# Performance work log

Measured on AMD Instinct MI355X. Metric: run time of the kernel, lower is better.

Reference implementation:

```python
import jax, jax.numpy as jnp
import numpy as np

EPS = 1e-5


def sage_conv(x, src, dst, Wl, Wr, b, n):
    # PyG SAGEConv: out_i = W_l * mean_{j in N(i)} x_j + W_r * x_i + b
    agg = jax.ops.segment_sum(x[src], dst, num_segments=n)  # [N, d]
    deg = jax.ops.segment_sum(jnp.ones_like(src, dtype=x.dtype), dst, num_segments=n)
    agg = agg / jnp.maximum(deg, 1.0)[:, None]
    return agg @ Wl + x @ Wr + b


def setup_inputs() -> dict:
    key = jax.random.key(0)
    ks = jax.random.split(key, 12)
    N, E, D_IN, D_H, D_OUT = 50000, 600000, 128, 128, 64
    x = jax.random.normal(ks[0], (N, D_IN), dtype=jnp.float32)
    edge_index = jax.random.randint(ks[1], (2, E), 0, N, dtype=jnp.int64)
    s_in = 1.0 / np.sqrt(D_IN)
    s_h = 1.0 / np.sqrt(D_H)
    return {
        "x": x,
        "edge_index": edge_index,
        "Wl0": jax.random.normal(ks[2], (D_IN, D_H), jnp.float32) * s_in,
        "Wr0": jax.random.normal(ks[3], (D_IN, D_H), jnp.float32) * s_in,
        "b0": jnp.zeros((D_H,), jnp.float32),
        "Wl1": jax.random.normal(ks[4], (D_H, D_H), jnp.float32) * s_h,
        "Wr1": jax.random.normal(ks[5], (D_H, D_H), jnp.float32) * s_h,
        "b1": jnp.zeros((D_H,), jnp.float32),
        "Wl2": jax.random.normal(ks[6], (D_H, D_OUT), jnp.float32) * s_h,
        "Wr2": jax.random.normal(ks[7], (D_H, D_OUT), jnp.float32) * s_h,
        "b2": jnp.zeros((D_OUT,), jnp.float32),
        "gamma": jnp.ones((D_H,), jnp.float32),
        "beta": jnp.zeros((D_H,), jnp.float32),
    }


def reference(x, edge_index, Wl0, Wr0, b0, Wl1, Wr1, b1, Wl2, Wr2, b2, gamma, beta):
    n = x.shape[0]
    src, dst = edge_index[0], edge_index[1]
    residual = x  # in_channels == hidden_channels -> no residual_transform
    # layer 0: conv + relu (+ dropout as identity in eval)
    h = jax.nn.relu(sage_conv(x, src, dst, Wl0, Wr0, b0, n))
    # middle layer: conv + BN(batch stats) + relu + residual
    h = sage_conv(h, src, dst, Wl1, Wr1, b1, n)
    mu = jnp.mean(h, axis=0)
    var = jnp.var(h, axis=0)  # biased, as in torch BN normalization
    h = (h - mu) * jax.lax.rsqrt(var + EPS) * gamma + beta
    h = jax.nn.relu(h) + residual
    # output layer
    h = sage_conv(h, src, dst, Wl2, Wr2, b2, n)
    return jax.nn.log_softmax(h, axis=-1)
```

## Files before the change

### kernel.cpp

```cpp
#include <hip/hip_runtime.h>
#include <hip/hip_bf16.h>


#define WS_EPS 1e-5f

typedef unsigned short ushort_t;
typedef unsigned int uint_t;
typedef unsigned char uchar_t;
typedef ushort_t ushort8 __attribute__((ext_vector_type(8)));
typedef short short8 __attribute__((ext_vector_type(8)));
typedef float f32x4 __attribute__((ext_vector_type(4)));
typedef _Float16 half2v __attribute__((ext_vector_type(2)));

__device__ __forceinline__ float bf2f(ushort_t u) {
    return __uint_as_float(((uint_t)u) << 16);
}
__device__ __forceinline__ ushort_t f2bf(float f) {
    uint_t u = __float_as_uint(f);
    u = (u + 0x7fffu + ((u >> 16) & 1u)) >> 16;
    return (ushort_t)u;
}
__device__ __forceinline__ uchar_t f2e4m3(float f) {
    _Float16 hf = (_Float16)f;
    uint_t h = (uint_t)__builtin_bit_cast(unsigned short, hf);
    uint_t s = (h >> 8) & 0x80u;
    uint_t r = h & 0x7fffu;
    if (r < 0x2400u) return (uchar_t)0;
    if (r > 0x5F40u) r = 0x5F00u;
    uint_t u = r - 0x2000u;
    uint_t m = (u + 0x3fu + ((u >> 7) & 1u)) >> 7;
    return (uchar_t)(s | m);
}

constexpr int SCHUNK = 4096;

__global__ __launch_bounds__(256) void k_scan_part(const int* __restrict__ deg,
                                                   int* __restrict__ bsum, int n) {
    int t = threadIdx.x;
    int base = blockIdx.x * SCHUNK + t * 16;
    int s = 0;
#pragma unroll
    for (int j = 0; j < 16; ++j) {
        int i = base + j;
        if (i < n) s += deg[i];
    }
#pragma unroll
    for (int d = 1; d < 64; d <<= 1) s += __shfl_xor(s, d);
    __shared__ int wt[4];
    if ((t & 63) == 0) wt[t >> 6] = s;
    __syncthreads();
    if (t == 0) bsum[blockIdx.x] = wt[0] + wt[1] + wt[2] + wt[3];
}

__global__ __launch_bounds__(64) void k_scan_bsum(const int* __restrict__ bsum,
                                                  int* __restrict__ boff,
                                                  int* __restrict__ off_n, int nb) {
    int lane = threadIdx.x;
    int carry = 0;
    for (int base = 0; base < nb; base += 64) {
        int t = base + lane;
        int v = (t < nb) ? bsum[t] : 0;
        int x = v;
#pragma unroll
        for (int d = 1; d < 64; d <<= 1) {
            int y = __shfl_up(x, d);
            if (lane >= d) x += y;
        }
        if (t < nb) boff[t] = carry + x - v;
        carry += __shfl(x, 63);
    }
    if (lane == 0) *off_n = carry;
}

__global__ __launch_bounds__(256) void k_scan_apply(const int* __restrict__ deg,
                                                    const int* __restrict__ boff,
                                                    int* __restrict__ off, int n) {
    int t = threadIdx.x;
    int lane = t & 63, wid = t >> 6;
    int base = blockIdx.x * SCHUNK + t * 16;
    int v[16];
    int s = 0;
#pragma unroll
    for (int j = 0; j < 16; ++j) {
        int i = base + j;
        v[j] = (i < n) ? deg[i] : 0;
        s += v[j];
    }
    int x = s;
#pragma unroll
    for (int d = 1; d < 64; d <<= 1) {
        int y = __shfl_up(x, d);
        if (lane >= d) x += y;
    }
    __shared__ int wtot[4];
    if (lane == 63) wtot[wid] = x;
    __syncthreads();
    int woff = 0;
    for (int wj = 0; wj < wid; ++wj) woff += wtot[wj];
    int run = boff[blockIdx.x] + woff + x - s;
#pragma unroll
    for (int j = 0; j < 16; ++j) {
        int i = base + j;
        if (i < n) off[i] = run;
        run += v[j];
    }
}

__global__ __launch_bounds__(256) void k_scatter(const int* __restrict__ ei,
                                                 const int* __restrict__ off,
                                                 int* __restrict__ cur,
                                                 int* __restrict__ csr, int E) {
    int e = blockIdx.x * 256 + threadIdx.x;
    if (e < E) {
        int d = ei[E + e];
        int s = ei[e];
        int p = atomicAdd(&cur[d], 1);
        csr[off[d] + p] = s;
    }
}

__global__ __launch_bounds__(256) void k_deg_prep(const int* __restrict__ ei,
                                                  int* __restrict__ deg, int E, int eb,
                                                  const float* __restrict__ x,
                                                  ushort_t* __restrict__ xb,
                                                  uchar_t* __restrict__ x8,
                                                  int total2, int nb_cvt,
                                                  const float* __restrict__ Wl0,
                                                  const float* __restrict__ Wr0,
                                                  const float* __restrict__ Wl1,
                                                  const float* __restrict__ Wr1,
                                                  const float* __restrict__ Wl2,
                                                  const float* __restrict__ Wr2,
                                                  ushort_t* __restrict__ wts) {
    int b = blockIdx.x;
    if (b < eb) {
        int e = b * 256 + threadIdx.x;
        if (e < E) atomicAdd(&deg[ei[E + e]], 1);
        return;
    }
    b -= eb;
    if (b < nb_cvt) {
        int i = b * 256 + threadIdx.x;
        if (i >= total2) return;
        float2 v = *(const float2*)&x[(size_t)i * 2];
        uint_t p = (uint_t)f2bf(v.x) | ((uint_t)f2bf(v.y) << 16);
        *(uint_t*)&xb[(size_t)i * 2] = p;
        ushort_t q = (ushort_t)((uint_t)f2e4m3(v.x) | ((uint_t)f2e4m3(v.y) << 8));
        *(ushort_t*)&x8[(size_t)i * 2] = q;
        return;
    }
    int id = (b - nb_cvt) * 256 + threadIdx.x;
    if (id >= 81920) return;
    const float* W;
    int rel, nout, base;
    if (id < 65536) {
        int m = id >> 14;
        rel = id & 16383;
        nout = 128;
        base = m << 14;
        W = (m == 0) ? Wl0 : (m == 1) ? Wr0 : (m == 2) ? Wl1 : Wr1;
    } else {
        int m = (id - 65536) >> 13;
        rel = (id - 65536) & 8191;
        nout = 64;
        base = 65536 + (m << 13);
        W = (m == 0) ? Wl2 : Wr2;
    }
    int c = rel >> 7;
    int k = rel & 127;
    wts[base + rel] = f2bf(W[(size_t)k * nout + c]);
}

constexpr int LDK = 136;

template <int EPI>
__global__ __launch_bounds__(256, 2) void k_dgemm(const ushort_t* __restrict__ X1,
                                                  const ushort_t* __restrict__ W1,
                                                  const ushort_t* __restrict__ X2,
                                                  const ushort_t* __restrict__ W2,
                                                  const float* __restrict__ bias,
                                                  ushort_t* __restrict__ outp,
                                                  uchar_t* __restrict__ out8,
                                                  float* __restrict__ stats, int n) {
    constexpr int K = 128, NOUT = 128;
    __shared__ ushort_t Bs[2 * 64 * LDK];

    const int t = threadIdx.x;
    const int lane = t & 63;
    const int r16 = lane & 15, kb = lane >> 4;
    const int colbase = (blockIdx.x & 1) * 64;

#pragma unroll
    for (int u = 0; u < 8; ++u) {
        int f = u * 256 + t;
        int rel = f & 1023;
        int col = rel >> 4, seg = rel & 15;
        const ushort_t* Wm = (u < 4) ? W1 : W2;
        *(ushort8*)&Bs[(u < 4 ? 0 : 1) * 64 * LDK + col * LDK + seg * 8] =
            *(const ushort8*)&Wm[(size_t)(colbase + col) * K + seg * 8];
    }
    __syncthreads();

    float bcol[4];
#pragma unroll
    for (int fn = 0; fn < 4; ++fn) bcol[fn] = bias[colbase + fn * 16 + r16];
    float ssum[4] = {0.f, 0.f, 0.f, 0.f}, qsum[4] = {0.f, 0.f, 0.f, 0.f};

    const int strips = (n + 15) >> 4;
    const int wstr = (gridDim.x >> 1) * 4;
    const int s0 = (blockIdx.x >> 1) * 4 + (t >> 6);

    auto loadA = [&](short8* a, int s) {
        int arow = s * 16 + r16;
        bool ok = arow < n;
        size_t xo = (size_t)arow * K + kb * 8;
#pragma unroll
        for (int ks = 0; ks < 4; ++ks)
            a[ks] = ok ? *(const short8*)&X1[xo + ks * 32] : (short8)0;
#pragma unroll
        for (int ks = 0; ks < 4; ++ks)
            a[4 + ks] = ok ? *(const short8*)&X2[xo + ks * 32] : (short8)0;
    };

    auto work = [&](const short8* a, int s) {
        f32x4 acc[4] = {(f32x4)0.f, (f32x4)0.f, (f32x4)0.f, (f32x4)0.f};
#pragma unroll
        for (int ks = 0; ks < 4; ++ks) {
#pragma unroll
            for (int fn = 0; fn < 4; ++fn) {
                short8 b = *(const short8*)&Bs[(fn * 16 + r16) * LDK + ks * 32 + kb * 8];
                acc[fn] = __builtin_amdgcn_mfma_f32_16x16x32_bf16(a[ks], b, acc[fn], 0, 0, 0);
            }
        }
#pragma unroll
        for (int ks = 0; ks < 4; ++ks) {
#pragma unroll
            for (int fn = 0; fn < 4; ++fn) {
                short8 b = *(const short8*)&Bs[64 * LDK + (fn * 16 + r16) * LDK + ks * 32 + kb * 8];
                acc[fn] = __builtin_amdgcn_mfma_f32_16x16x32_bf16(a[4 + ks], b, acc[fn], 0, 0, 0);
            }
        }
        int rb = s * 16 + kb * 4;
#pragma unroll
        for (int r = 0; r < 4; ++r) {
            int row = rb + r;
            if (row >= n) continue;
#pragma unroll
            for (int fn = 0; fn < 4; ++fn) {
                int col = colbase + fn * 16 + r16;
                float v = acc[fn][r] + bcol[fn];
                if constexpr (EPI == 2) {
                    float rv = fmaxf(v, 0.f);
                    outp[(size_t)row * NOUT + col] = f2bf(rv);
                    out8[(size_t)row * NOUT + col] = f2e4m3(rv);
                } else {
                    outp[(size_t)row * NOUT + col] = f2bf(v);
                    ssum[fn] += v;
                    qsum[fn] += v * v;
                }
            }
        }
    };

    short8 aA[8], aB[8], aC[8];
    int s = s0;
    if (s < strips) {
        loadA(aA, s);
        int sB = s + wstr;
        bool vB = sB < strips;
        if (vB) loadA(aB, sB);
        for (;;) {
            int sC = sB + wstr;
            bool vC = vB && (sC < strips);
            if (vC) loadA(aC, sC);
            work(aA, s);
            if (!vB) break;
            int sD = sC + wstr;
            bool vD = vC && (sD < strips);
            if (vD) loadA(aA, sD);
            work(aB, sB);
            if (!vC) break;
            int sE = sD + wstr;
            bool vE = vD && (sE < strips);
            if (vE) loadA(aB, sE);
            work(aC, sC);
            if (!vD) break;
            s = sD;
            sB = sE;
            vB = vE;
        }
    }

    if constexpr (EPI == 1) {
#pragma unroll
        for (int fn = 0; fn < 4; ++fn) {
            ssum[fn] += __shfl_xor(ssum[fn], 16);
            ssum[fn] += __shfl_xor(ssum[fn], 32);
            qsum[fn] += __shfl_xor(qsum[fn], 16);
            qsum[fn] += __shfl_xor(qsum[fn], 32);
        }
        if (kb == 0) {
#pragma unroll
            for (int fn = 0; fn < 4; ++fn) {
                int col = colbase + fn * 16 + r16;
                atomicAdd(&stats[col], ssum[fn]);
                atomicAdd(&stats[128 + col], qsum[fn]);
            }
        }
    }
}

__global__ __launch_bounds__(256, 2) void k_cgemm(const ushort_t* __restrict__ H,
                                                  const ushort_t* __restrict__ WL,
                                                  const ushort_t* __restrict__ WR,
                                                  const float* __restrict__ b2,
                                                  ushort_t* __restrict__ A64,
                                                  ushort_t* __restrict__ Tb, int n) {
    constexpr int K = 128;
    __shared__ ushort_t Bs[2 * 64 * LDK];

    const int t = threadIdx.x;
    const int lane = t & 63;
    const int r16 = lane & 15, kb = lane >> 4;

#pragma unroll
    for (int u = 0; u < 8; ++u) {
        int f = u * 256 + t;
        int rel = f & 1023;
        int col = rel >> 4, seg = rel & 15;
        const ushort_t* Wm = (u < 4) ? WL : WR;
        *(ushort8*)&Bs[(u < 4 ? 0 : 1) * 64 * LDK + col * LDK + seg * 8] =
            *(const ushort8*)&Wm[(size_t)col * K + seg * 8];
    }
    __syncthreads();

    float bcol[4];
#pragma unroll
    for (int fn = 0; fn < 4; ++fn) bcol[fn] = b2[fn * 16 + r16];

    const int strips = (n + 15) >> 4;
    const int wstr = gridDim.x * 4;
    const int s0 = blockIdx.x * 4 + (t >> 6);

    auto loadA = [&](short8* a, int s) {
        int arow = s * 16 + r16;
        bool ok = arow < n;
        size_t xo = (size_t)arow * K + kb * 8;
#pragma unroll
        for (int ks = 0; ks < 4; ++ks)
            a[ks] = ok ? *(const short8*)&H[xo + ks * 32] : (short8)0;
    };

    auto work = [&](const short8* a, int s) {
        f32x4 aL[4] = {(f32x4)0.f, (f32x4)0.f, (f32x4)0.f, (f32x4)0.f};
        f32x4 aR[4] = {(f32x4)0.f, (f32x4)0.f, (f32x4)0.f, (f32x4)0.f};
#pragma unroll
        for (int ks = 0; ks < 4; ++ks) {
#pragma unroll
            for (int fn = 0; fn < 4; ++fn) {
                short8 bl = *(const short8*)&Bs[(fn * 16 + r16) * LDK + ks * 32 + kb * 8];
                short8 br = *(const short8*)&Bs[64 * LDK + (fn * 16 + r16) * LDK + ks * 32 + kb * 8];
                aL[fn] = __builtin_amdgcn_mfma_f32_16x16x32_bf16(a[ks], bl, aL[fn], 0, 0, 0);
                aR[fn] = __builtin_amdgcn_mfma_f32_16x16x32_bf16(a[ks], br, aR[fn], 0, 0, 0);
            }
        }
        int rb = s * 16 + kb * 4;
#pragma unroll
        for (int r = 0; r < 4; ++r) {
            int row = rb + r;
            if (row >= n) continue;
#pragma unroll
            for (int fn = 0; fn < 4; ++fn) {
                int col = fn * 16 + r16;
                A64[(size_t)row * 64 + col] = f2bf(aL[fn][r]);
                Tb[(size_t)row * 64 + col] = f2bf(aR[fn][r] + bcol[fn]);
            }
        }
    };

    short8 aA[4], aB[4], aC[4];
    int s = s0;
    if (s < strips) {
        loadA(aA, s);
        int sB = s + wstr;
        bool vB = sB < strips;
        if (vB) loadA(aB, sB);
        for (;;) {
            int sC = sB + wstr;
            bool vC = vB && (sC < strips);
            if (vC) loadA(aC, sC);
            work(aA, s);
            if (!vB) break;
            int sD = sC + wstr;
            bool vD = vC && (sD < strips);
            if (vD) loadA(aA, sD);
            work(aB, sB);
            if (!vC) break;
            int sE = sD + wstr;
            bool vE = vD && (sE < strips);
            if (vE) loadA(aB, sE);
            work(aC, sC);
            if (!vD) break;
            s = sD;
            sB = sE;
            vB = vE;
        }
    }
}

__global__ __launch_bounds__(256) void k_segmean8(const uchar_t* __restrict__ U8,
                                                  const int* __restrict__ off,
                                                  const int* __restrict__ srcs,
                                                  ushort_t* __restrict__ out, int n) {
    int node = blockIdx.x * 32 + (threadIdx.x >> 3);
    int sub = threadIdx.x & 7;
    if (node >= n) return;
    int beg = off[node], end = off[node + 1];
    half2v aE0 = (half2v)0, aE1 = (half2v)0, aE2 = (half2v)0, aE3 = (half2v)0;
    half2v aO0 = (half2v)0, aO1 = (half2v)0, aO2 = (half2v)0, aO3 = (half2v)0;

#define DEC(dw, AE, AO)                                                           \
    {                                                                             \
        uint_t xe = (dw)&0x00ff00ffu;                                             \
        uint_t xo = ((dw) >> 8) & 0x00ff00ffu;                                    \
        uint_t he = ((xe & 0x00800080u) << 8) |                                   \
                    (((xe & 0x007f007fu) << 7) + 0x20002000u);                    \
        uint_t ho = ((xo & 0x00800080u) << 8) |                                   \
                    (((xo & 0x007f007fu) << 7) + 0x20002000u);                    \
        AE += __builtin_bit_cast(half2v, he);                                     \
        AO += __builtin_bit_cast(half2v, ho);                                     \
    }

    auto addrow = [&](int sidx) {
        uint4 v = *(const uint4*)&U8[(size_t)sidx * 128 + sub * 16];
        DEC(v.x, aE0, aO0)
        DEC(v.y, aE1, aO1)
        DEC(v.z, aE2, aO2)
        DEC(v.w, aE3, aO3)
    };
#undef DEC

    int i = beg;
    for (; i + 8 <= end; i += 8) {
        int sv[8];
#pragma unroll
        for (int u = 0; u < 8; ++u) sv[u] = srcs[i + u];
#pragma unroll
        for (int u = 0; u < 8; ++u) addrow(sv[u]);
    }
    for (; i < end; ++i) addrow(srcs[i]);

    int d = end - beg;
    float inv = 1.f / (float)(d > 1 ? d : 1);
    ushort8 o0, o1;
#define PACK(AE, AO, O, IDX)                     \
    O[IDX] = f2bf((float)AE[0] * inv);           \
    O[IDX + 1] = f2bf((float)AO[0] * inv);       \
    O[IDX + 2] = f2bf((float)AE[1] * inv);       \
    O[IDX + 3] = f2bf((float)AO[1] * inv);
    PACK(aE0, aO0, o0, 0)
    PACK(aE1, aO1, o0, 4)
    PACK(aE2, aO2, o1, 0)
    PACK(aE3, aO3, o1, 4)
#undef PACK
    *(ushort8*)&out[(size_t)node * 128 + sub * 16] = o0;
    *(ushort8*)&out[(size_t)node * 128 + sub * 16 + 8] = o1;
}

__global__ __launch_bounds__(256) void k_segmean_lsm(const ushort_t* __restrict__ A64,
                                                     const int* __restrict__ off,
                                                     const int* __restrict__ srcs,
                                                     const ushort_t* __restrict__ Tb,
                                                     float* __restrict__ out, int n) {
    int node = blockIdx.x * 32 + (threadIdx.x >> 3);
    int sub = threadIdx.x & 7;
    if (node >= n) return;
    int beg = off[node], end = off[node + 1];
    float a[8];
#pragma unroll
    for (int j = 0; j < 8; ++j) a[j] = 0.f;
    int i = beg;
    for (; i + 8 <= end; i += 8) {
        int sv[8];
#pragma unroll
        for (int u = 0; u < 8; ++u) sv[u] = srcs[i + u];
#pragma unroll
        for (int u = 0; u < 8; ++u) {
            ushort8 v = *(const ushort8*)&A64[(size_t)sv[u] * 64 + sub * 8];
#pragma unroll
            for (int j = 0; j < 8; ++j) a[j] += bf2f((ushort_t)v[j]);
        }
    }
    for (; i < end; ++i) {
        ushort8 v = *(const ushort8*)&A64[(size_t)srcs[i] * 64 + sub * 8];
#pragma unroll
        for (int j = 0; j < 8; ++j) a[j] += bf2f((ushort_t)v[j]);
    }
    int d = end - beg;
    float inv = 1.f / (float)(d > 1 ? d : 1);
    ushort8 tv = *(const ushort8*)&Tb[(size_t)node * 64 + sub * 8];
    float vv[8];
#pragma unroll
    for (int j = 0; j < 8; ++j) vv[j] = a[j] * inv + bf2f((ushort_t)tv[j]);
    float m = vv[0];
#pragma unroll
    for (int j = 1; j < 8; ++j) m = fmaxf(m, vv[j]);
#pragma unroll
    for (int dd = 1; dd < 8; dd <<= 1) m = fmaxf(m, __shfl_xor(m, dd));
    float e = 0.f;
#pragma unroll
    for (int j = 0; j < 8; ++j) e += expf(vv[j] - m);
#pragma unroll
    for (int dd = 1; dd < 8; dd <<= 1) e += __shfl_xor(e, dd);
    float lg = m + logf(e);
    f32x4 o0, o1;
#pragma unroll
    for (int j = 0; j < 4; ++j) {
        o0[j] = vv[j] - lg;
        o1[j] = vv[4 + j] - lg;
    }
    *(f32x4*)&out[(size_t)node * 64 + sub * 8] = o0;
    *(f32x4*)&out[(size_t)node * 64 + sub * 8 + 4] = o1;
}

__global__ __launch_bounds__(256) void k_bnapply(const ushort_t* __restrict__ P,
                                                 const ushort_t* __restrict__ Xb,
                                                 const float* __restrict__ stats,
                                                 const float* __restrict__ gamma,
                                                 const float* __restrict__ beta,
                                                 ushort_t* __restrict__ H, int n) {
    int i = blockIdx.x * 256 + threadIdx.x;
    if (i >= n * 64) return;
    int nd = i >> 6;
    int c = (i & 63) << 1;
    float inv_n = 1.f / (float)n;
    float mu0 = stats[c] * inv_n, mu1 = stats[c + 1] * inv_n;
    float v0 = stats[128 + c] * inv_n - mu0 * mu0;
    float v1 = stats[128 + c + 1] * inv_n - mu1 * mu1;
    float s0 = rsqrtf(v0 + WS_EPS) * gamma[c];
    float s1 = rsqrtf(v1 + WS_EPS) * gamma[c + 1];
    uint_t pv = *(const uint_t*)&P[(size_t)nd * 128 + c];
    uint_t xv = *(const uint_t*)&Xb[(size_t)nd * 128 + c];
    float p0 = __uint_as_float(pv << 16);
    float p1 = __uint_as_float(pv & 0xffff0000u);
    float x0 = __uint_as_float(xv << 16);
    float x1 = __uint_as_float(xv & 0xffff0000u);
    float h0 = fmaxf((p0 - mu0) * s0 + beta[c], 0.f) + x0;
    float h1 = fmaxf((p1 - mu1) * s1 + beta[c + 1], 0.f) + x1;
    uint_t pk = (uint_t)f2bf(h0) | ((uint_t)f2bf(h1) << 16);
    *(uint_t*)&H[(size_t)nd * 128 + c] = pk;
}

extern "C" void kernel_launch(void* const* d_in, const int* in_sizes, int n_in,
                              void* d_out, int out_size, void* d_ws, size_t ws_size,
                              hipStream_t stream) {
    const float* x     = (const float*)d_in[0];
    const int*   ei    = (const int*)d_in[1];
    const float* Wl0   = (const float*)d_in[2];
    const float* Wr0   = (const float*)d_in[3];
    const float* b0    = (const float*)d_in[4];
    const float* Wl1   = (const float*)d_in[5];
    const float* Wr1   = (const float*)d_in[6];
    const float* b1    = (const float*)d_in[7];
    const float* Wl2   = (const float*)d_in[8];
    const float* Wr2   = (const float*)d_in[9];
    const float* b2    = (const float*)d_in[10];
    const float* gamma = (const float*)d_in[11];
    const float* beta  = (const float*)d_in[12];

    const int n = in_sizes[0] / 128;
    const int E = in_sizes[1] / 2;
    const int nb_scan = (n + SCHUNK - 1) / SCHUNK;

    char* w = (char*)d_ws;
    auto alloc = [&](size_t bytes) -> void* {
        void* p = (void*)w;
        w += (bytes + 255) & ~(size_t)255;
        return p;
    };
    int*      deg   = (int*)alloc((size_t)n * 4);
    int*      cur   = (int*)alloc((size_t)n * 4);
    float*    stats = (float*)alloc(256 * 4);
    size_t    zbytes = (size_t)((char*)w - (char*)deg);
    int*      off   = (int*)alloc(((size_t)n + 1) * 4);
    int*      csr   = (int*)alloc((size_t)E * 4);
    int*      bsum  = (int*)alloc(256 * 4);
    int*      boff  = (int*)alloc(256 * 4);
    ushort_t* wts   = (ushort_t*)alloc((size_t)81920 * 2);
    ushort_t* xb    = (ushort_t*)alloc((size_t)n * 128 * 2);
    uchar_t*  x8    = (uchar_t*)alloc((size_t)n * 128);
    ushort_t* H     = (ushort_t*)alloc((size_t)n * 128 * 2);
    uchar_t*  H8    = (uchar_t*)alloc((size_t)n * 128);
    ushort_t* Pb    = (ushort_t*)alloc((size_t)n * 128 * 2);
    ushort_t* M     = (ushort_t*)alloc((size_t)n * 128 * 2);
    ushort_t* A64   = (ushort_t*)alloc((size_t)n * 64 * 2);
    ushort_t* Tb    = (ushort_t*)alloc((size_t)n * 64 * 2);

    ushort_t* WtL0 = wts;
    ushort_t* WtR0 = wts + 16384;
    ushort_t* WtL1 = wts + 32768;
    ushort_t* WtR1 = wts + 49152;
    ushort_t* WtL2 = wts + 65536;
    ushort_t* WtR2 = wts + 73728;

    hipMemsetAsync(deg, 0, zbytes, stream);

    const int eb = (E + 255) / 256;
    const int nb_cvt = (n * 64 + 255) / 256;
    k_deg_prep<<<eb + nb_cvt + 320, 256, 0, stream>>>(ei, deg, E, eb, x, xb, x8,
                                                      n * 64, nb_cvt,
                                                      Wl0, Wr0, Wl1, Wr1, Wl2, Wr2, wts);
    k_scan_part<<<nb_scan, 256, 0, stream>>>(deg, bsum, n);
    k_scan_bsum<<<1, 64, 0, stream>>>(bsum, boff, off + n, nb_scan);
    k_scan_apply<<<nb_scan, 256, 0, stream>>>(deg, boff, off, n);
    k_scatter<<<(E + 255) / 256, 256, 0, stream>>>(ei, off, cur, csr, E);

    const int GB_D = 512;
    const int GB_C = 256;
    const int smb = (n + 31) / 32;

    k_segmean8<<<smb, 256, 0, stream>>>(x8, off, csr, M, n);
    k_dgemm<2><<<GB_D, 256, 0, stream>>>(xb, WtR0, M, WtL0, b0, H, H8, nullptr, n);

    k_segmean8<<<smb, 256, 0, stream>>>(H8, off, csr, M, n);
    k_dgemm<1><<<GB_D, 256, 0, stream>>>(H, WtR1, M, WtL1, b1, Pb, nullptr, stats, n);
    k_bnapply<<<(n * 64 + 255) / 256, 256, 0, stream>>>(Pb, xb, stats, gamma, beta, H, n);

    k_cgemm<<<GB_C, 256, 0, stream>>>(H, WtL2, WtR2, b2, A64, Tb, n);
    k_segmean_lsm<<<smb, 256, 0, stream>>>(A64, off, csr, Tb, (float*)d_out, n);
}
```

Before: 243.0 us.

## Replace persistent LDS-staged GEMMs with one-strip-per-wave register-held weights

The dense GEMM kernels drop the LDS staging of weights and the persistent, triple-buffered strip loop. Each wave now handles a single 16-row strip and loads its weight fragments straight from global memory into registers, and the grid is sized to the number of strips. This removes the LDS traffic, the block barrier and the loop bookkeeping. In exchange, every wave re-reads the weights (served mostly from cache), register pressure rises, and far more blocks are launched with no overlap of loads and compute inside a wave. The BN stats atomics also become per-wave, so there are many more of them.

```diff
diff --git a/kernel.cpp b/kernel.cpp
--- a/kernel.cpp
+++ b/kernel.cpp
@@ -171,8 +171,6 @@
     wts[base + rel] = f2bf(W[(size_t)k * nout + c]);
 }
 
-constexpr int LDK = 136;
-
 template <int EPI>
 __global__ __launch_bounds__(256, 2) void k_dgemm(const ushort_t* __restrict__ X1,
                                                   const ushort_t* __restrict__ W1,
@@ -183,64 +181,56 @@
                                                   uchar_t* __restrict__ out8,
                                                   float* __restrict__ stats, int n) {
     constexpr int K = 128, NOUT = 128;
-    __shared__ ushort_t Bs[2 * 64 * LDK];
-
     const int t = threadIdx.x;
     const int lane = t & 63;
     const int r16 = lane & 15, kb = lane >> 4;
-    const int colbase = (blockIdx.x & 1) * 64;
-
-#pragma unroll
-    for (int u = 0; u < 8; ++u) {
-        int f = u * 256 + t;
-        int rel = f & 1023;
-        int col = rel >> 4, seg = rel & 15;
-        const ushort_t* Wm = (u < 4) ? W1 : W2;
-        *(ushort8*)&Bs[(u < 4 ? 0 : 1) * 64 * LDK + col * LDK + seg * 8] =
-            *(const ushort8*)&Wm[(size_t)(colbase + col) * K + seg * 8];
-    }
-    __syncthreads();
+    const int w = t >> 6;
+    const int strip = blockIdx.x * 2 + (w >> 1);
+    const int colbase = (w & 1) * 64;
+    const int strips = (n + 15) >> 4;
+    if (strip >= strips) return;
+
+    short8 B1[4][4], B2[4][4];
+#pragma unroll
+    for (int fn = 0; fn < 4; ++fn)
+#pragma unroll
+        for (int ks = 0; ks < 4; ++ks)
+            B1[fn][ks] = *(const short8*)&W1[(size_t)(colbase + fn * 16 + r16) * K + ks * 32 + kb * 8];
+#pragma unroll
+    for (int fn = 0; fn < 4; ++fn)
+#pragma unroll
+        for (int ks = 0; ks < 4; ++ks)
+            B2[fn][ks] = *(const short8*)&W2[(size_t)(colbase + fn * 16 + r16) * K + ks * 32 + kb * 8];
+
+    const int arow = strip * 16 + r16;
+    const bool rok = (arow < n);
+    const size_t xo = (size_t)arow * K + kb * 8;
+    short8 a1[4], a2[4];
+#pragma unroll
+    for (int ks = 0; ks < 4; ++ks)
+        a1[ks] = rok ? *(const short8*)&X1[xo + ks * 32] : (short8)0;
+#pragma unroll
+    for (int ks = 0; ks < 4; ++ks)
+        a2[ks] = rok ? *(const short8*)&X2[xo + ks * 32] : (short8)0;
+
+    f32x4 acc[4] = {(f32x4)0.f, (f32x4)0.f, (f32x4)0.f, (f32x4)0.f};
+#pragma unroll
+    for (int ks = 0; ks < 4; ++ks)
+#pragma unroll
+        for (int fn = 0; fn < 4; ++fn)
+            acc[fn] = __builtin_amdgcn_mfma_f32_16x16x32_bf16(a1[ks], B1[fn][ks], acc[fn], 0, 0, 0);
+#pragma unroll
+    for (int ks = 0; ks < 4; ++ks)
+#pragma unroll
+        for (int fn = 0; fn < 4; ++fn)
+            acc[fn] = __builtin_amdgcn_mfma_f32_16x16x32_bf16(a2[ks], B2[fn][ks], acc[fn], 0, 0, 0);
 
     float bcol[4];
 #pragma unroll
     for (int fn = 0; fn < 4; ++fn) bcol[fn] = bias[colbase + fn * 16 + r16];
-    float ssum[4] = {0.f, 0.f, 0.f, 0.f}, qsum[4] = {0.f, 0.f, 0.f, 0.f};
-
-    const int strips = (n + 15) >> 4;
-    const int wstr = (gridDim.x >> 1) * 4;
-    const int s0 = (blockIdx.x >> 1) * 4 + (t >> 6);
-
-    auto loadA = [&](short8* a, int s) {
-        int arow = s * 16 + r16;
-        bool ok = arow < n;
-        size_t xo = (size_t)arow * K + kb * 8;
-#pragma unroll
-        for (int ks = 0; ks < 4; ++ks)
-            a[ks] = ok ? *(const short8*)&X1[xo + ks * 32] : (short8)0;
-#pragma unroll
-        for (int ks = 0; ks < 4; ++ks)
-            a[4 + ks] = ok ? *(const short8*)&X2[xo + ks * 32] : (short8)0;
-    };
-
-    auto work = [&](const short8* a, int s) {
-        f32x4 acc[4] = {(f32x4)0.f, (f32x4)0.f, (f32x4)0.f, (f32x4)0.f};
-#pragma unroll
-        for (int ks = 0; ks < 4; ++ks) {
-#pragma unroll
-            for (int fn = 0; fn < 4; ++fn) {
-                short8 b = *(const short8*)&Bs[(fn * 16 + r16) * LDK + ks * 32 + kb * 8];
-                acc[fn] = __builtin_amdgcn_mfma_f32_16x16x32_bf16(a[ks], b, acc[fn], 0, 0, 0);
-            }
-        }
-#pragma unroll
-        for (int ks = 0; ks < 4; ++ks) {
-#pragma unroll
-            for (int fn = 0; fn < 4; ++fn) {
-                short8 b = *(const short8*)&Bs[64 * LDK + (fn * 16 + r16) * LDK + ks * 32 + kb * 8];
-                acc[fn] = __builtin_amdgcn_mfma_f32_16x16x32_bf16(a[4 + ks], b, acc[fn], 0, 0, 0);
-            }
-        }
-        int rb = s * 16 + kb * 4;
+
+    if constexpr (EPI == 2) {
+        const int rb = strip * 16 + kb * 4;
 #pragma unroll
         for (int r = 0; r < 4; ++r) {
             int row = rb + r;
@@ -248,50 +238,27 @@
 #pragma unroll
             for (int fn = 0; fn < 4; ++fn) {
                 int col = colbase + fn * 16 + r16;
+                float v = fmaxf(acc[fn][r] + bcol[fn], 0.f);
+                outp[(size_t)row * NOUT + col] = f2bf(v);
+                out8[(size_t)row * NOUT + col] = f2e4m3(v);
+            }
+        }
+    } else {
+        float ssum[4] = {0.f, 0.f, 0.f, 0.f}, qsum[4] = {0.f, 0.f, 0.f, 0.f};
+        const int rb = strip * 16 + kb * 4;
+#pragma unroll
+        for (int r = 0; r < 4; ++r) {
+            int row = rb + r;
+            if (row >= n) continue;
+#pragma unroll
+            for (int fn = 0; fn < 4; ++fn) {
+                int col = colbase + fn * 16 + r16;
                 float v = acc[fn][r] + bcol[fn];
-                if constexpr (EPI == 2) {
-                    float rv = fmaxf(v, 0.f);
-                    outp[(size_t)row * NOUT + col] = f2bf(rv);
-                    out8[(size_t)row * NOUT + col] = f2e4m3(rv);
-                } else {
-                    outp[(size_t)row * NOUT + col] = f2bf(v);
-                    ssum[fn] += v;
-                    qsum[fn] += v * v;
-                }
+                outp[(size_t)row * NOUT + col] = f2bf(v);
+                ssum[fn] += v;
+                qsum[fn] += v * v;
             }
         }
-    };
-
-    short8 aA[8], aB[8], aC[8];
-    int s = s0;
-    if (s < strips) {
-        loadA(aA, s);
-        int sB = s + wstr;
-        bool vB = sB < strips;
-        if (vB) loadA(aB, sB);
-        for (;;) {
-            int sC = sB + wstr;
-            bool vC = vB && (sC < strips);
-            if (vC) loadA(aC, sC);
-            work(aA, s);
-            if (!vB) break;
-            int sD = sC + wstr;
-            bool vD = vC && (sD < strips);
-            if (vD) loadA(aA, sD);
-            work(aB, sB);
-            if (!vC) break;
-            int sE = sD + wstr;
-            bool vE = vD && (sE < strips);
-            if (vE) loadA(aB, sE);
-            work(aC, sC);
-            if (!vD) break;
-            s = sD;
-            sB = sE;
-            vB = vE;
-        }
-    }
-
-    if constexpr (EPI == 1) {
 #pragma unroll
         for (int fn = 0; fn < 4; ++fn) {
             ssum[fn] += __shfl_xor(ssum[fn], 16);
@@ -317,93 +284,57 @@
                                                   ushort_t* __restrict__ A64,
                                                   ushort_t* __restrict__ Tb, int n) {
     constexpr int K = 128;
-    __shared__ ushort_t Bs[2 * 64 * LDK];
-
     const int t = threadIdx.x;
     const int lane = t & 63;
     const int r16 = lane & 15, kb = lane >> 4;
-
-#pragma unroll
-    for (int u = 0; u < 8; ++u) {
-        int f = u * 256 + t;
-        int rel = f & 1023;
-        int col = rel >> 4, seg = rel & 15;
-        const ushort_t* Wm = (u < 4) ? WL : WR;
-        *(ushort8*)&Bs[(u < 4 ? 0 : 1) * 64 * LDK + col * LDK + seg * 8] =
-            *(const ushort8*)&Wm[(size_t)col * K + seg * 8];
-    }
-    __syncthreads();
+    const int strip = blockIdx.x * 4 + (t >> 6);
+    const int strips = (n + 15) >> 4;
+    if (strip >= strips) return;
+
+    short8 BL[4][4], BR[4][4];
+#pragma unroll
+    for (int fn = 0; fn < 4; ++fn)
+#pragma unroll
+        for (int ks = 0; ks < 4; ++ks)
+            BL[fn][ks] = *(const short8*)&WL[(size_t)(fn * 16 + r16) * K + ks * 32 + kb * 8];
+#pragma unroll
+    for (int fn = 0; fn < 4; ++fn)
+#pragma unroll
+        for (int ks = 0; ks < 4; ++ks)
+            BR[fn][ks] = *(const short8*)&WR[(size_t)(fn * 16 + r16) * K + ks * 32 + kb * 8];
+
+    const int arow = strip * 16 + r16;
+    const bool rok = (arow < n);
+    const size_t xo = (size_t)arow * K + kb * 8;
+    short8 a[4];
+#pragma unroll
+    for (int ks = 0; ks < 4; ++ks)
+        a[ks] = rok ? *(const short8*)&H[xo + ks * 32] : (short8)0;
+
+    f32x4 aL[4] = {(f32x4)0.f, (f32x4)0.f, (f32x4)0.f, (f32x4)0.f};
+    f32x4 aR[4] = {(f32x4)0.f, (f32x4)0.f, (f32x4)0.f, (f32x4)0.f};
+#pragma unroll
+    for (int ks = 0; ks < 4; ++ks)
+#pragma unroll
+        for (int fn = 0; fn < 4; ++fn) {
+            aL[fn] = __builtin_amdgcn_mfma_f32_16x16x32_bf16(a[ks], BL[fn][ks], aL[fn], 0, 0, 0);
+            aR[fn] = __builtin_amdgcn_mfma_f32_16x16x32_bf16(a[ks], BR[fn][ks], aR[fn], 0, 0, 0);
+        }
 
     float bcol[4];
 #pragma unroll
     for (int fn = 0; fn < 4; ++fn) bcol[fn] = b2[fn * 16 + r16];
 
-    const int strips = (n + 15) >> 4;
-    const int wstr = gridDim.x * 4;
-    const int s0 = blockIdx.x * 4 + (t >> 6);
-
-    auto loadA = [&](short8* a, int s) {
-        int arow = s * 16 + r16;
-        bool ok = arow < n;
-        size_t xo = (size_t)arow * K + kb * 8;
-#pragma unroll
-        for (int ks = 0; ks < 4; ++ks)
-            a[ks] = ok ? *(const short8*)&H[xo + ks * 32] : (short8)0;
-    };
-
-    auto work = [&](const short8* a, int s) {
-        f32x4 aL[4] = {(f32x4)0.f, (f32x4)0.f, (f32x4)0.f, (f32x4)0.f};
-        f32x4 aR[4] = {(f32x4)0.f, (f32x4)0.f, (f32x4)0.f, (f32x4)0.f};
-#pragma unroll
-        for (int ks = 0; ks < 4; ++ks) {
-#pragma unroll
-            for (int fn = 0; fn < 4; ++fn) {
-                short8 bl = *(const short8*)&Bs[(fn * 16 + r16) * LDK + ks * 32 + kb * 8];
-                short8 br = *(const short8*)&Bs[64 * LDK + (fn * 16 + r16) * LDK + ks * 32 + kb * 8];
-                aL[fn] = __builtin_amdgcn_mfma_f32_16x16x32_bf16(a[ks], bl, aL[fn], 0, 0, 0);
-                aR[fn] = __builtin_amdgcn_mfma_f32_16x16x32_bf16(a[ks], br, aR[fn], 0, 0, 0);
-            }
-        }
-        int rb = s * 16 + kb * 4;
-#pragma unroll
-        for (int r = 0; r < 4; ++r) {
-            int row = rb + r;
-            if (row >= n) continue;
-#pragma unroll
-            for (int fn = 0; fn < 4; ++fn) {
-                int col = fn * 16 + r16;
-                A64[(size_t)row * 64 + col] = f2bf(aL[fn][r]);
-                Tb[(size_t)row * 64 + col] = f2bf(aR[fn][r] + bcol[fn]);
-            }
-        }
-    };
-
-    short8 aA[4], aB[4], aC[4];
-    int s = s0;
-    if (s < strips) {
-        loadA(aA, s);
-        int sB = s + wstr;
-        bool vB = sB < strips;
-        if (vB) loadA(aB, sB);
-        for (;;) {
-            int sC = sB + wstr;
-            bool vC = vB && (sC < strips);
-            if (vC) loadA(aC, sC);
-            work(aA, s);
-            if (!vB) break;
-            int sD = sC + wstr;
-            bool vD = vC && (sD < strips);
-            if (vD) loadA(aA, sD);
-            work(aB, sB);
-            if (!vC) break;
-            int sE = sD + wstr;
-            bool vE = vD && (sE < strips);
-            if (vE) loadA(aB, sE);
-            work(aC, sC);
-            if (!vD) break;
-            s = sD;
-            sB = sE;
-            vB = vE;
+    const int rb = strip * 16 + kb * 4;
+#pragma unroll
+    for (int r = 0; r < 4; ++r) {
+        int row = rb + r;
+        if (row >= n) continue;
+#pragma unroll
+        for (int fn = 0; fn < 4; ++fn) {
+            int col = fn * 16 + r16;
+            A64[(size_t)row * 64 + col] = f2bf(aL[fn][r]);
+            Tb[(size_t)row * 64 + col] = f2bf(aR[fn][r] + bcol[fn]);
         }
     }
 }
@@ -615,17 +546,18 @@
     k_scan_apply<<<nb_scan, 256, 0, stream>>>(deg, boff, off, n);
     k_scatter<<<(E + 255) / 256, 256, 0, stream>>>(ei, off, cur, csr, E);
 
-    const int GB_D = 512;
-    const int GB_C = 256;
+    const int strips = (n + 15) / 16;
+    const int gb_d = (strips + 1) / 2;
+    const int gb_c = (strips + 3) / 4;
     const int smb = (n + 31) / 32;
 
     k_segmean8<<<smb, 256, 0, stream>>>(x8, off, csr, M, n);
-    k_dgemm<2><<<GB_D, 256, 0, stream>>>(xb, WtR0, M, WtL0, b0, H, H8, nullptr, n);
+    k_dgemm<2><<<gb_d, 256, 0, stream>>>(xb, WtR0, M, WtL0, b0, H, H8, nullptr, n);
 
     k_segmean8<<<smb, 256, 0, stream>>>(H8, off, csr, M, n);
-    k_dgemm<1><<<GB_D, 256, 0, stream>>>(H, WtR1, M, WtL1, b1, Pb, nullptr, stats, n);
+    k_dgemm<1><<<gb_d, 256, 0, stream>>>(H, WtR1, M, WtL1, b1, Pb, nullptr, stats, n);
     k_bnapply<<<(n * 64 + 255) / 256, 256, 0, stream>>>(Pb, xb, stats, gamma, beta, H, n);
 
-    k_cgemm<<<GB_C, 256, 0, stream>>>(H, WtL2, WtR2, b2, A64, Tb, n);
+    k_cgemm<<<gb_c, 256, 0, stream>>>(H, WtL2, WtR2, b2, A64, Tb, n);
     k_segmean_lsm<<<smb, 256, 0, stream>>>(A64, off, csr, Tb, (float*)d_out, n);
 }
```

After: 307.3 us. 26.5% more time.
